# Kernel optimization log

Hardware: AMD Instinct MI355X
Metric: run time of the kernel (lower is better)

The kernel has to match this reference:

```python
import jax, jax.numpy as jnp
import numpy as np

B, N, C = 32, 4096, 768
H = 12
D = C // H  # head_dim = 64
SCALE = D ** -0.5


def setup_inputs() -> dict:
    key = jax.random.key(0)
    ks = jax.random.split(key, 9)
    s = 0.02
    return {
        "x": jax.random.normal(ks[0], (B, N, C), dtype=jnp.float32),
        "Wq": jax.random.normal(ks[1], (C, C), dtype=jnp.float32) * s,
        "bq": jnp.zeros((C,), dtype=jnp.float32),
        "Wk": jax.random.normal(ks[2], (C, C), dtype=jnp.float32) * s,
        "bk": jnp.zeros((C,), dtype=jnp.float32),
        "Wv": jax.random.normal(ks[3], (C, C), dtype=jnp.float32) * s,
        "bv": jnp.zeros((C,), dtype=jnp.float32),
        "Wp": jax.random.normal(ks[4], (C, C), dtype=jnp.float32) * s,
        "bp": jnp.zeros((C,), dtype=jnp.float32),
    }


def reference(x, Wq, bq, Wk, bk, Wv, bv, Wp, bp):
    b, n, c = x.shape
    # q from CLS token only -> (B, H, 1, D), pre-scaled
    q = (x[:, 0] @ Wq + bq).reshape(b, 1, H, D).transpose(0, 2, 1, 3) * SCALE
    # k, v from all tokens -> (B, H, N, D)
    k = (x @ Wk + bk).reshape(b, n, H, D).transpose(0, 2, 1, 3)
    v = (x @ Wv + bv).reshape(b, n, H, D).transpose(0, 2, 1, 3)
    # attention scores (B, H, 1, N), stable softmax over keys
    attn = jax.nn.softmax(jnp.einsum("bhqd,bhnd->bhqn", q, k), axis=-1)
    # weighted sum over values -> (B, H, 1, D) -> (B, 1, C)
    x_cls = jnp.einsum("bhqn,bhnd->bhqd", attn, v)
    x_cls = x_cls.transpose(0, 2, 1, 3).reshape(b, 1, c)
    x_cls = x_cls @ Wp + bp
    return x_cls, attn
```

## Files before the change

### kernel.cpp

```cpp
#include <hip/hip_runtime.h>

#define BB 32
#define NN 4096
#define CC 768
#define HH 12
#define DD 64
#define QSCALE 0.125f
#define NCHUNK 32

#define OFF_Q       0
#define OFF_SB      24576
#define OFF_U       24960
#define OFF_WPART   319872
#define OFF_XCLSPRE 9757056

__global__ __launch_bounds__(256) void k_q(const float* __restrict__ x,
                                           const float* __restrict__ Wq,
                                           const float* __restrict__ bq,
                                           float* __restrict__ q) {
    int bh = blockIdx.x;
    int b = bh / HH, h = bh % HH;
    int t = threadIdx.x;
    int d = t & 63, cg = t >> 6;
    int col = h * DD + d;
    const float* xr = x + (size_t)b * NN * CC;
    float acc = 0.f;
    #pragma unroll 8
    for (int c = cg * 192; c < cg * 192 + 192; ++c)
        acc += xr[c] * Wq[(size_t)c * CC + col];
    __shared__ float red[256];
    red[t] = acc;
    __syncthreads();
    if (t < 64) {
        float v = red[t] + red[t + 64] + red[t + 128] + red[t + 192];
        q[bh * DD + d] = (v + bq[col]) * QSCALE;
    }
}

__global__ __launch_bounds__(256) void k_U(const float* __restrict__ Wk,
                                           const float* __restrict__ bk,
                                           const float* __restrict__ q,
                                           float* __restrict__ U,
                                           float* __restrict__ sb) {
    int bh = blockIdx.x;
    int h = bh % HH;
    __shared__ float qs[DD];
    int t = threadIdx.x;
    if (t < DD) qs[t] = q[bh * DD + t];
    __syncthreads();
    for (int c = t; c < CC; c += 256) {
        const float4* wr = (const float4*)(Wk + (size_t)c * CC + h * DD);
        float acc = 0.f;
        #pragma unroll
        for (int d4 = 0; d4 < DD / 4; ++d4) {
            float4 wv = wr[d4];
            acc += wv.x * qs[4 * d4] + wv.y * qs[4 * d4 + 1]
                 + wv.z * qs[4 * d4 + 2] + wv.w * qs[4 * d4 + 3];
        }
        U[(size_t)bh * CC + c] = acc;
    }
    if (t == 0) {
        float acc = 0.f;
        for (int d = 0; d < DD; ++d) acc += qs[d] * bk[h * DD + d];
        sb[bh] = acc;
    }
}

__global__ __launch_bounds__(512) void k_scores(const float* __restrict__ x,
                                                const float* __restrict__ U,
                                                const float* __restrict__ sb,
                                                float* __restrict__ scores) {
    int b = blockIdx.x >> 5, chunk = blockIdx.x & 31;
    int n0 = chunk * 128;
    __shared__ float4 U4[HH * 192];
    __shared__ float sbs[HH];
    int t = threadIdx.x;
    const float4* Ug = (const float4*)(U + (size_t)b * HH * CC);
    for (int i = t; i < HH * 192; i += 512) U4[i] = Ug[i];
    if (t < HH) sbs[t] = sb[b * HH + t];
    __syncthreads();
    int w = t >> 6, l = t & 63;
    #pragma unroll 2
    for (int i = 0; i < 16; ++i) {
        int n = n0 + i * 8 + w;
        const float4* xr = (const float4*)(x + ((size_t)b * NN + n) * CC);
        float4 a0 = xr[l], a1 = xr[l + 64], a2 = xr[l + 128];
        float acc[HH];
        #pragma unroll
        for (int h = 0; h < HH; ++h) {
            float4 u0 = U4[h * 192 + l];
            float4 u1 = U4[h * 192 + 64 + l];
            float4 u2 = U4[h * 192 + 128 + l];
            acc[h] = a0.x * u0.x + a0.y * u0.y + a0.z * u0.z + a0.w * u0.w
                   + a1.x * u1.x + a1.y * u1.y + a1.z * u1.z + a1.w * u1.w
                   + a2.x * u2.x + a2.y * u2.y + a2.z * u2.z + a2.w * u2.w;
        }
        #pragma unroll
        for (int h = 0; h < HH; ++h) {
            float v = acc[h];
            #pragma unroll
            for (int m = 32; m; m >>= 1) v += __shfl_xor(v, m, 64);
            acc[h] = v;
        }
        float outv = 0.f;
        #pragma unroll
        for (int h = 0; h < HH; ++h)
            if (l == h) outv = acc[h];
        if (l < HH)
            scores[((size_t)b * HH + l) * NN + n] = outv + sbs[l];
    }
}

__global__ __launch_bounds__(256) void k_softmax(float* __restrict__ attn) {
    int bh = blockIdx.x;
    float4* row = (float4*)(attn + (size_t)bh * NN);
    int t = threadIdx.x;
    float4 v[4];
    #pragma unroll
    for (int i = 0; i < 4; ++i) v[i] = row[t + 256 * i];
    float m = -1e30f;
    #pragma unroll
    for (int i = 0; i < 4; ++i)
        m = fmaxf(m, fmaxf(fmaxf(v[i].x, v[i].y), fmaxf(v[i].z, v[i].w)));
    #pragma unroll
    for (int mm = 32; mm; mm >>= 1) m = fmaxf(m, __shfl_xor(m, mm, 64));
    __shared__ float redm[4], reds[4];
    int w = t >> 6, l = t & 63;
    if (l == 0) redm[w] = m;
    __syncthreads();
    m = fmaxf(fmaxf(redm[0], redm[1]), fmaxf(redm[2], redm[3]));
    float s = 0.f;
    #pragma unroll
    for (int i = 0; i < 4; ++i) {
        v[i].x = __expf(v[i].x - m); v[i].y = __expf(v[i].y - m);
        v[i].z = __expf(v[i].z - m); v[i].w = __expf(v[i].w - m);
        s += v[i].x + v[i].y + v[i].z + v[i].w;
    }
    #pragma unroll
    for (int mm = 32; mm; mm >>= 1) s += __shfl_xor(s, mm, 64);
    if (l == 0) reds[w] = s;
    __syncthreads();
    float inv = 1.f / (reds[0] + reds[1] + reds[2] + reds[3]);
    #pragma unroll
    for (int i = 0; i < 4; ++i) {
        v[i].x *= inv; v[i].y *= inv; v[i].z *= inv; v[i].w *= inv;
        row[t + 256 * i] = v[i];
    }
}

#define FMA4(A, s, X) { (A).x += (s)*(X).x; (A).y += (s)*(X).y; (A).z += (s)*(X).z; (A).w += (s)*(X).w; }
__global__ __launch_bounds__(192) void k_wpart(const float* __restrict__ x,
                                               const float* __restrict__ attn,
                                               float* __restrict__ wpart) {
    int b = blockIdx.x >> 5, chunk = blockIdx.x & 31;
    int n0 = chunk * 128;
    __shared__ float al[128][HH];
    int t = threadIdx.x;
    const float* ag = attn + (size_t)b * HH * NN + n0;
    for (int i = t; i < HH * 128; i += 192) {
        int h = i >> 7, n = i & 127;
        al[n][h] = ag[(size_t)h * NN + n];
    }
    __syncthreads();
    float4 acc[HH];
    #pragma unroll
    for (int h = 0; h < HH; ++h) acc[h] = make_float4(0.f, 0.f, 0.f, 0.f);
    const float4* xb = (const float4*)(x + ((size_t)b * NN + n0) * CC);
    #pragma unroll 4
    for (int n = 0; n < 128; ++n) {
        float4 xv = xb[(size_t)n * 192 + t];
        float4 a0 = *(const float4*)&al[n][0];
        float4 a1 = *(const float4*)&al[n][4];
        float4 a2 = *(const float4*)&al[n][8];
        FMA4(acc[0],  a0.x, xv); FMA4(acc[1],  a0.y, xv);
        FMA4(acc[2],  a0.z, xv); FMA4(acc[3],  a0.w, xv);
        FMA4(acc[4],  a1.x, xv); FMA4(acc[5],  a1.y, xv);
        FMA4(acc[6],  a1.z, xv); FMA4(acc[7],  a1.w, xv);
        FMA4(acc[8],  a2.x, xv); FMA4(acc[9],  a2.y, xv);
        FMA4(acc[10], a2.z, xv); FMA4(acc[11], a2.w, xv);
    }
    float4* wp = (float4*)(wpart + (((size_t)b * NCHUNK + chunk) * HH) * CC);
    #pragma unroll
    for (int h = 0; h < HH; ++h)
        wp[h * 192 + t] = acc[h];
}

__global__ __launch_bounds__(256) void k_xcls1(const float* __restrict__ wpart,
                                               const float* __restrict__ Wv,
                                               const float* __restrict__ bv,
                                               float* __restrict__ xclspre) {
    int bh = blockIdx.x, b = bh / HH, h = bh % HH;
    __shared__ float wl[CC];
    __shared__ float red[256];
    int t = threadIdx.x;
    for (int c = t; c < CC; c += 256) {
        float s = 0.f;
        #pragma unroll
        for (int ch = 0; ch < NCHUNK; ++ch)
            s += wpart[(((size_t)b * NCHUNK + ch) * HH + h) * CC + c];
        wl[c] = s;
    }
    __syncthreads();
    int d = t & 63, cg = t >> 6;
    int col = h * DD + d;
    float acc = 0.f;
    #pragma unroll 8
    for (int c = cg * 192; c < cg * 192 + 192; ++c)
        acc += wl[c] * Wv[(size_t)c * CC + col];
    red[t] = acc;
    __syncthreads();
    if (t < 64)
        xclspre[b * CC + col] = red[t] + red[t + 64] + red[t + 128] + red[t + 192] + bv[col];
}

__global__ __launch_bounds__(256) void k_proj(const float* __restrict__ xclspre,
                                              const float* __restrict__ Wp,
                                              const float* __restrict__ bp,
                                              float* __restrict__ out) {
    int blk = blockIdx.x, b = blk / 12, jg = blk % 12;
    __shared__ float xs[CC];
    __shared__ float red[256];
    int t = threadIdx.x;
    for (int c = t; c < CC; c += 256) xs[c] = xclspre[b * CC + c];
    __syncthreads();
    int d = t & 63, cg = t >> 6;
    int j = jg * DD + d;
    float acc = 0.f;
    #pragma unroll 8
    for (int c = cg * 192; c < cg * 192 + 192; ++c)
        acc += xs[c] * Wp[(size_t)c * CC + j];
    red[t] = acc;
    __syncthreads();
    if (t < 64)
        out[b * CC + j] = red[t] + red[t + 64] + red[t + 128] + red[t + 192] + bp[j];
}

extern "C" void kernel_launch(void* const* d_in, const int* in_sizes, int n_in,
                              void* d_out, int out_size, void* d_ws, size_t ws_size,
                              hipStream_t stream) {
    const float* x  = (const float*)d_in[0];
    const float* Wq = (const float*)d_in[1];
    const float* bq = (const float*)d_in[2];
    const float* Wk = (const float*)d_in[3];
    const float* bk = (const float*)d_in[4];
    const float* Wv = (const float*)d_in[5];
    const float* bv = (const float*)d_in[6];
    const float* Wp = (const float*)d_in[7];
    const float* bp = (const float*)d_in[8];
    float* out = (float*)d_out;
    float* ws  = (float*)d_ws;

    float* q       = ws + OFF_Q;
    float* sb      = ws + OFF_SB;
    float* U       = ws + OFF_U;
    float* wpart   = ws + OFF_WPART;
    float* xclspre = ws + OFF_XCLSPRE;

    float* xcls = out;
    float* attn = out + BB * CC;

    hipLaunchKernelGGL(k_q,       dim3(BB * HH), dim3(256), 0, stream, x, Wq, bq, q);
    hipLaunchKernelGGL(k_U,       dim3(BB * HH), dim3(256), 0, stream, Wk, bk, q, U, sb);
    hipLaunchKernelGGL(k_scores,  dim3(BB * 32), dim3(512), 0, stream, x, U, sb, attn);
    hipLaunchKernelGGL(k_softmax, dim3(BB * HH), dim3(256), 0, stream, attn);
    hipLaunchKernelGGL(k_wpart,   dim3(BB * NCHUNK), dim3(192), 0, stream, x, attn, wpart);
    hipLaunchKernelGGL(k_xcls1,   dim3(BB * HH), dim3(256), 0, stream, wpart, Wv, bv, xclspre);
    hipLaunchKernelGGL(k_proj,    dim3(BB * 12), dim3(256), 0, stream, xclspre, Wp, bp, xcls);
}
```

Baseline: 702.0 us.

## Fuse q and U kernels, double rows in scores, finer wpart chunks with separate reduction

Merges the q projection and U computation into one kernel so q stays in shared memory and one launch is dropped. The scores kernel now has each warp process two rows per iteration, reusing each shared-memory U load for two dot products. k_wpart splits N into 64 chunks instead of 32 for more blocks, and the cross-chunk sum moves into a new fully parallel k_wsum kernel instead of running serially inside k_xcls. This doubles the wpart workspace traffic and adds a launch, in exchange for more parallelism.

```diff
diff --git a/kernel.cpp b/kernel.cpp
--- a/kernel.cpp
+++ b/kernel.cpp
@@ -6,63 +6,55 @@
 #define HH 12
 #define DD 64
 #define QSCALE 0.125f
-#define NCHUNK 32
-
-#define OFF_Q       0
-#define OFF_SB      24576
-#define OFF_U       24960
-#define OFF_WPART   319872
-#define OFF_XCLSPRE 9757056
-
-__global__ __launch_bounds__(256) void k_q(const float* __restrict__ x,
-                                           const float* __restrict__ Wq,
-                                           const float* __restrict__ bq,
-                                           float* __restrict__ q) {
+#define NCHUNK 64
+
+#define OFF_SB      0
+#define OFF_U       384
+#define OFF_WPART   295296
+#define OFF_W       19169664
+#define OFF_XCLSPRE 19464576
+
+__global__ __launch_bounds__(256) void k_qU(const float* __restrict__ x,
+                                            const float* __restrict__ Wq,
+                                            const float* __restrict__ bq,
+                                            const float* __restrict__ Wk,
+                                            const float* __restrict__ bk,
+                                            float* __restrict__ U,
+                                            float* __restrict__ sb) {
     int bh = blockIdx.x;
     int b = bh / HH, h = bh % HH;
     int t = threadIdx.x;
     int d = t & 63, cg = t >> 6;
     int col = h * DD + d;
+    __shared__ float red[256];
+    __shared__ float qs[DD];
     const float* xr = x + (size_t)b * NN * CC;
     float acc = 0.f;
     #pragma unroll 8
     for (int c = cg * 192; c < cg * 192 + 192; ++c)
         acc += xr[c] * Wq[(size_t)c * CC + col];
-    __shared__ float red[256];
     red[t] = acc;
     __syncthreads();
     if (t < 64) {
         float v = red[t] + red[t + 64] + red[t + 128] + red[t + 192];
-        q[bh * DD + d] = (v + bq[col]) * QSCALE;
-    }
-}
-
-__global__ __launch_bounds__(256) void k_U(const float* __restrict__ Wk,
-                                           const float* __restrict__ bk,
-                                           const float* __restrict__ q,
-                                           float* __restrict__ U,
-                                           float* __restrict__ sb) {
-    int bh = blockIdx.x;
-    int h = bh % HH;
-    __shared__ float qs[DD];
-    int t = threadIdx.x;
-    if (t < DD) qs[t] = q[bh * DD + t];
+        qs[t] = (v + bq[col]) * QSCALE;
+    }
     __syncthreads();
     for (int c = t; c < CC; c += 256) {
         const float4* wr = (const float4*)(Wk + (size_t)c * CC + h * DD);
-        float acc = 0.f;
+        float a = 0.f;
         #pragma unroll
         for (int d4 = 0; d4 < DD / 4; ++d4) {
             float4 wv = wr[d4];
-            acc += wv.x * qs[4 * d4] + wv.y * qs[4 * d4 + 1]
-                 + wv.z * qs[4 * d4 + 2] + wv.w * qs[4 * d4 + 3];
-        }
-        U[(size_t)bh * CC + c] = acc;
+            a += wv.x * qs[4 * d4] + wv.y * qs[4 * d4 + 1]
+               + wv.z * qs[4 * d4 + 2] + wv.w * qs[4 * d4 + 3];
+        }
+        U[(size_t)bh * CC + c] = a;
     }
     if (t == 0) {
-        float acc = 0.f;
-        for (int d = 0; d < DD; ++d) acc += qs[d] * bk[h * DD + d];
-        sb[bh] = acc;
+        float a = 0.f;
+        for (int d2 = 0; d2 < DD; ++d2) a += qs[d2] * bk[h * DD + d2];
+        sb[bh] = a;
     }
 }
 
@@ -81,33 +73,43 @@
     __syncthreads();
     int w = t >> 6, l = t & 63;
     #pragma unroll 2
-    for (int i = 0; i < 16; ++i) {
-        int n = n0 + i * 8 + w;
-        const float4* xr = (const float4*)(x + ((size_t)b * NN + n) * CC);
-        float4 a0 = xr[l], a1 = xr[l + 64], a2 = xr[l + 128];
-        float acc[HH];
+    for (int i = 0; i < 8; ++i) {
+        int n = n0 + i * 16 + w * 2;
+        const float4* xr0 = (const float4*)(x + ((size_t)b * NN + n) * CC);
+        const float4* xr1 = xr0 + 192;
+        float4 a0[3], a1[3];
+        a0[0] = xr0[l]; a0[1] = xr0[l + 64]; a0[2] = xr0[l + 128];
+        a1[0] = xr1[l]; a1[1] = xr1[l + 64]; a1[2] = xr1[l + 128];
+        float acc0[HH], acc1[HH];
+        #pragma unroll
+        for (int h = 0; h < HH; ++h) { acc0[h] = 0.f; acc1[h] = 0.f; }
+        #pragma unroll
+        for (int k = 0; k < 3; ++k) {
+            #pragma unroll
+            for (int h = 0; h < HH; ++h) {
+                float4 u = U4[h * 192 + k * 64 + l];
+                acc0[h] += u.x * a0[k].x + u.y * a0[k].y + u.z * a0[k].z + u.w * a0[k].w;
+                acc1[h] += u.x * a1[k].x + u.y * a1[k].y + u.z * a1[k].z + u.w * a1[k].w;
+            }
+        }
         #pragma unroll
         for (int h = 0; h < HH; ++h) {
-            float4 u0 = U4[h * 192 + l];
-            float4 u1 = U4[h * 192 + 64 + l];
-            float4 u2 = U4[h * 192 + 128 + l];
-            acc[h] = a0.x * u0.x + a0.y * u0.y + a0.z * u0.z + a0.w * u0.w
-                   + a1.x * u1.x + a1.y * u1.y + a1.z * u1.z + a1.w * u1.w
-                   + a2.x * u2.x + a2.y * u2.y + a2.z * u2.z + a2.w * u2.w;
-        }
-        #pragma unroll
-        for (int h = 0; h < HH; ++h) {
-            float v = acc[h];
+            float v0 = acc0[h], v1 = acc1[h];
             #pragma unroll
-            for (int m = 32; m; m >>= 1) v += __shfl_xor(v, m, 64);
-            acc[h] = v;
-        }
-        float outv = 0.f;
+            for (int m = 32; m; m >>= 1) {
+                v0 += __shfl_xor(v0, m, 64);
+                v1 += __shfl_xor(v1, m, 64);
+            }
+            acc0[h] = v0; acc1[h] = v1;
+        }
+        float out0 = 0.f, out1 = 0.f;
         #pragma unroll
         for (int h = 0; h < HH; ++h)
-            if (l == h) outv = acc[h];
-        if (l < HH)
-            scores[((size_t)b * HH + l) * NN + n] = outv + sbs[l];
+            if (l == h) { out0 = acc0[h]; out1 = acc1[h]; }
+        if (l < HH) {
+            scores[((size_t)b * HH + l) * NN + n]     = out0 + sbs[l];
+            scores[((size_t)b * HH + l) * NN + n + 1] = out1 + sbs[l];
+        }
     }
 }
 
@@ -152,13 +154,13 @@
 __global__ __launch_bounds__(192) void k_wpart(const float* __restrict__ x,
                                                const float* __restrict__ attn,
                                                float* __restrict__ wpart) {
-    int b = blockIdx.x >> 5, chunk = blockIdx.x & 31;
-    int n0 = chunk * 128;
-    __shared__ float al[128][HH];
+    int b = blockIdx.x >> 6, chunk = blockIdx.x & 63;
+    int n0 = chunk * 64;
+    __shared__ float al[64][HH];
     int t = threadIdx.x;
     const float* ag = attn + (size_t)b * HH * NN + n0;
-    for (int i = t; i < HH * 128; i += 192) {
-        int h = i >> 7, n = i & 127;
+    for (int i = t; i < HH * 64; i += 192) {
+        int h = i >> 6, n = i & 63;
         al[n][h] = ag[(size_t)h * NN + n];
     }
     __syncthreads();
@@ -166,8 +168,8 @@
     #pragma unroll
     for (int h = 0; h < HH; ++h) acc[h] = make_float4(0.f, 0.f, 0.f, 0.f);
     const float4* xb = (const float4*)(x + ((size_t)b * NN + n0) * CC);
-    #pragma unroll 4
-    for (int n = 0; n < 128; ++n) {
+    #pragma unroll 2
+    for (int n = 0; n < 64; ++n) {
         float4 xv = xb[(size_t)n * 192 + t];
         float4 a0 = *(const float4*)&al[n][0];
         float4 a1 = *(const float4*)&al[n][4];
@@ -185,7 +187,19 @@
         wp[h * 192 + t] = acc[h];
 }
 
-__global__ __launch_bounds__(256) void k_xcls1(const float* __restrict__ wpart,
+__global__ __launch_bounds__(256) void k_wsum(const float* __restrict__ wpart,
+                                              float* __restrict__ w) {
+    int i = blockIdx.x * 256 + threadIdx.x;
+    int b = i / (HH * CC), r = i - b * (HH * CC);
+    const float* p = wpart + (size_t)b * NCHUNK * HH * CC + r;
+    float s = 0.f;
+    #pragma unroll 8
+    for (int ch = 0; ch < NCHUNK; ++ch)
+        s += p[(size_t)ch * HH * CC];
+    w[i] = s;
+}
+
+__global__ __launch_bounds__(256) void k_xcls2(const float* __restrict__ w,
                                                const float* __restrict__ Wv,
                                                const float* __restrict__ bv,
                                                float* __restrict__ xclspre) {
@@ -193,13 +207,7 @@
     __shared__ float wl[CC];
     __shared__ float red[256];
     int t = threadIdx.x;
-    for (int c = t; c < CC; c += 256) {
-        float s = 0.f;
-        #pragma unroll
-        for (int ch = 0; ch < NCHUNK; ++ch)
-            s += wpart[(((size_t)b * NCHUNK + ch) * HH + h) * CC + c];
-        wl[c] = s;
-    }
+    for (int c = t; c < CC; c += 256) wl[c] = w[(size_t)bh * CC + c];
     __syncthreads();
     int d = t & 63, cg = t >> 6;
     int col = h * DD + d;
@@ -250,20 +258,20 @@
     float* out = (float*)d_out;
     float* ws  = (float*)d_ws;
 
-    float* q       = ws + OFF_Q;
     float* sb      = ws + OFF_SB;
     float* U       = ws + OFF_U;
     float* wpart   = ws + OFF_WPART;
+    float* w       = ws + OFF_W;
     float* xclspre = ws + OFF_XCLSPRE;
 
     float* xcls = out;
     float* attn = out + BB * CC;
 
-    hipLaunchKernelGGL(k_q,       dim3(BB * HH), dim3(256), 0, stream, x, Wq, bq, q);
-    hipLaunchKernelGGL(k_U,       dim3(BB * HH), dim3(256), 0, stream, Wk, bk, q, U, sb);
+    hipLaunchKernelGGL(k_qU,      dim3(BB * HH), dim3(256), 0, stream, x, Wq, bq, Wk, bk, U, sb);
     hipLaunchKernelGGL(k_scores,  dim3(BB * 32), dim3(512), 0, stream, x, U, sb, attn);
     hipLaunchKernelGGL(k_softmax, dim3(BB * HH), dim3(256), 0, stream, attn);
     hipLaunchKernelGGL(k_wpart,   dim3(BB * NCHUNK), dim3(192), 0, stream, x, attn, wpart);
-    hipLaunchKernelGGL(k_xcls1,   dim3(BB * HH), dim3(256), 0, stream, wpart, Wv, bv, xclspre);
+    hipLaunchKernelGGL(k_wsum,    dim3(BB * HH * CC / 256), dim3(256), 0, stream, wpart, w);
+    hipLaunchKernelGGL(k_xcls2,   dim3(BB * HH), dim3(256), 0, stream, w, Wv, bv, xclspre);
     hipLaunchKernelGGL(k_proj,    dim3(BB * 12), dim3(256), 0, stream, xclspre, Wp, bp, xcls);
 }
```

After: 978.2 us. 1.39x slower.
